# Kernel optimization log

Hardware: AMD Instinct MI355X
Metric: run time of the kernel (lower is better)

The kernel has to match this reference:

```python
import jax, jax.numpy as jnp
import numpy as np

NUM_HEADS = 16
ROPE_THETA = 10000.0
SEQ = 2048
D_MODEL = 2048


def _rope(x):
    # x: (seq, heads, head_dim). Equinox RotaryPositionalEmbedding:
    # rotate_half variant with tiled (non-interleaved) cos/sin.
    S, H, hd = x.shape
    half = hd // 2
    freqs = 1.0 / (ROPE_THETA ** (jnp.arange(0, half, dtype=jnp.float32) * 2.0 / hd))  # (half,)
    t = jnp.arange(S, dtype=jnp.float32)
    angles = jnp.outer(t, freqs)  # (S, half)
    cos = jnp.tile(jnp.cos(angles), (1, 2))[:, None, :]  # (S, 1, hd)
    sin = jnp.tile(jnp.sin(angles), (1, 2))[:, None, :]
    x1, x2 = jnp.split(x, 2, axis=-1)
    rot = jnp.concatenate((-x2, x1), axis=-1)  # rotate_half
    return (x * cos + rot * sin).astype(x.dtype)


def setup_inputs() -> dict:
    key = jax.random.key(0)
    ks = jax.random.split(key, 7)
    mk = lambda k, scale=1.0: (jax.random.normal(k, (SEQ, D_MODEL), dtype=jnp.float32) * scale)
    return {
        "query": mk(ks[0]),
        "key_": mk(ks[1]),
        "value": mk(ks[2]),
        "Wq": jax.random.normal(ks[3], (D_MODEL, D_MODEL), dtype=jnp.float32) / np.sqrt(D_MODEL),
        "Wk": jax.random.normal(ks[4], (D_MODEL, D_MODEL), dtype=jnp.float32) / np.sqrt(D_MODEL),
        "Wv": jax.random.normal(ks[5], (D_MODEL, D_MODEL), dtype=jnp.float32) / np.sqrt(D_MODEL),
        "Wo": jax.random.normal(ks[6], (D_MODEL, D_MODEL), dtype=jnp.float32) / np.sqrt(D_MODEL),
    }


def reference(query, key_, value, Wq, Wk, Wv, Wo):
    S, D = query.shape
    H = NUM_HEADS
    hd = D // H
    # QKV projections (equinox Linear: y = W @ x, vmapped over seq -> x @ W.T)
    q = (query @ Wq.T).reshape(S, H, hd)
    k = (key_ @ Wk.T).reshape(S, H, hd)
    v = (value @ Wv.T).reshape(S, H, hd)
    # Per-head RoPE on q and k
    q = _rope(q)
    k = _rope(k)
    # Causal attention, scale 1/sqrt(head_dim) (dropout_p=0, inference)
    attn = jax.nn.dot_product_attention(q[None], k[None], v[None], is_causal=True)[0]  # (S, H, hd)
    # Output projection
    return attn.reshape(S, D) @ Wo.T
```

## Files before the change

kernel.cpp:

```cpp
#include <hip/hip_runtime.h>

typedef unsigned short u16;
typedef __attribute__((ext_vector_type(8))) __bf16 bf16x8;
typedef __attribute__((ext_vector_type(4))) float f32x4;

#define D_MODEL 2048
#define SEQ 2048
#define NHEAD 16
#define HDIM 128

#define AS1 __attribute__((address_space(1)))
#define AS3 __attribute__((address_space(3)))
#define GL2LDS(g, l) __builtin_amdgcn_global_load_lds((AS1 const void*)(g), (AS3 void*)(l), 16, 0, 0)

__device__ __forceinline__ u16 f2bf(float f) {
  unsigned u = __float_as_uint(f);
  u += 0x7fff + ((u >> 16) & 1);
  return (u16)(u >> 16);
}
__device__ __forceinline__ float bf2f(u16 h) {
  return __uint_as_float(((unsigned)h) << 16);
}
__device__ __forceinline__ float fexp2(float x) {
#if __has_builtin(__builtin_amdgcn_exp2f)
  return __builtin_amdgcn_exp2f(x);
#else
  return __expf(x * 0.69314718055994531f);
#endif
}

__global__ __launch_bounds__(256) void k_cast7(const float* i0, const float* i1, const float* i2,
                                               const float* i3, const float* i4, const float* i5,
                                               const float* i6,
                                               u16* o0, u16* o1, u16* o2, u16* o3, u16* o4,
                                               u16* o5, u16* o6) {
  const float* in; u16* out;
  switch (blockIdx.y) {
    case 0: in = i0; out = o0; break;
    case 1: in = i1; out = o1; break;
    case 2: in = i2; out = o2; break;
    case 3: in = i3; out = o3; break;
    case 4: in = i4; out = o4; break;
    case 5: in = i5; out = o5; break;
    default: in = i6; out = o6; break;
  }
  const int i = blockIdx.x * blockDim.x + threadIdx.x;
  const float4 v = reinterpret_cast<const float4*>(in)[i];
  ushort4 o;
  o.x = f2bf(v.x); o.y = f2bf(v.y); o.z = f2bf(v.z); o.w = f2bf(v.w);
  reinterpret_cast<ushort4*>(out)[i] = o;
}

__device__ __forceinline__ void stage128(const u16* __restrict__ P, u16* dst, int row0, int kt,
                                         int t, int w) {
#pragma unroll
  for (int c = 0; c < 4; ++c) {
    const int r = (c * 2048 + t * 8) >> 6;
    const int ch = ((t & 7) ^ (r & 7)) * 8;
    GL2LDS(P + (size_t)(row0 + r) * D_MODEL + kt + ch, dst + c * 2048 + w * 512);
  }
}
__device__ __forceinline__ void stage64(const u16* __restrict__ P, u16* dst, int row0, int kt,
                                        int t, int w) {
#pragma unroll
  for (int c = 0; c < 2; ++c) {
    const int r = (c * 2048 + t * 8) >> 6;
    const int ch = ((t & 7) ^ (r & 7)) * 8;
    GL2LDS(P + (size_t)(row0 + r) * D_MODEL + kt + ch, dst + c * 2048 + w * 512);
  }
}

__device__ __forceinline__ void gemm_nt_body(const u16* __restrict__ A, const u16* __restrict__ B,
                                             void* __restrict__ C, u16* As0, u16* As1,
                                             u16* Bs0, u16* Bs1, int outmode) {
  const int tn = blockIdx.x, tm = blockIdx.y;
  const int t = threadIdx.x;
  const int lane = t & 63, w = t >> 6;
  const int wr = w >> 1, wc = w & 1;
  const int lrow = lane & 15, g = lane >> 4;
  f32x4 acc[4][4] = {};

  stage128(A, As0, tm * 128, 0, t, w);
  stage128(B, Bs0, tn * 128, 0, t, w);
  __syncthreads();

  u16 *Ar = As0, *Br = Bs0, *Aw = As1, *Bw = Bs1;
#pragma unroll 1
  for (int kt = 0; kt < D_MODEL; kt += 64) {
    if (kt + 64 < D_MODEL) {
      stage128(A, Aw, tm * 128, kt + 64, t, w);
      stage128(B, Bw, tn * 128, kt + 64, t, w);
    }
#pragma unroll
    for (int kk = 0; kk < 2; ++kk) {
      bf16x8 af[4], bfr[4];
#pragma unroll
      for (int i = 0; i < 4; ++i) {
        const int sw = (((kk << 2) + g) ^ (lrow & 7)) * 8;
        af[i]  = *(const bf16x8*)(Ar + (wr * 64 + i * 16 + lrow) * 64 + sw);
        bfr[i] = *(const bf16x8*)(Br + (wc * 64 + i * 16 + lrow) * 64 + sw);
      }
#pragma unroll
      for (int i = 0; i < 4; ++i)
#pragma unroll
        for (int j = 0; j < 4; ++j)
          acc[i][j] = __builtin_amdgcn_mfma_f32_16x16x32_bf16(af[i], bfr[j], acc[i][j], 0, 0, 0);
    }
    __syncthreads();
    u16* tp;
    tp = Ar; Ar = Aw; Aw = tp;
    tp = Br; Br = Bw; Bw = tp;
  }

  const int crow0 = tm * 128 + wr * 64 + (lane >> 4) * 4;
  const int ccol0 = tn * 128 + wc * 64 + lrow;
  if (outmode == 2) {
#pragma unroll
    for (int i = 0; i < 4; ++i)
#pragma unroll
      for (int j = 0; j < 4; ++j) {
        ushort4 o;
        o.x = f2bf(acc[i][j][0]); o.y = f2bf(acc[i][j][1]);
        o.z = f2bf(acc[i][j][2]); o.w = f2bf(acc[i][j][3]);
        *(ushort4*)((u16*)C + (size_t)(ccol0 + j * 16) * D_MODEL + crow0 + i * 16) = o;
      }
  } else {
#pragma unroll
    for (int i = 0; i < 4; ++i)
#pragma unroll
      for (int j = 0; j < 4; ++j)
#pragma unroll
        for (int r = 0; r < 4; ++r)
          ((u16*)C)[(size_t)(crow0 + i * 16 + r) * D_MODEL + ccol0 + j * 16] = f2bf(acc[i][j][r]);
  }
}

__global__ __launch_bounds__(256, 2) void k_gemm_qkv(const u16* Xq, const u16* Xk, const u16* Xv,
                                                     const u16* Wq, const u16* Wk, const u16* Wv,
                                                     u16* Q, u16* K, u16* VT) {
  __shared__ u16 As[2][128 * 64], Bs[2][128 * 64];
  const int z = blockIdx.z;
  const u16* A = (z == 0) ? Xq : (z == 1) ? Xk : Xv;
  const u16* B = (z == 0) ? Wq : (z == 1) ? Wk : Wv;
  u16* C = (z == 0) ? Q : (z == 1) ? K : VT;
  gemm_nt_body(A, B, C, As[0], As[1], Bs[0], Bs[1], (z == 2) ? 2 : 0);
}

__global__ __launch_bounds__(256, 2) void k_gemm_out(const u16* __restrict__ A, const u16* __restrict__ B,
                                                     float* __restrict__ C) {
  __shared__ u16 As[2][128 * 64], Bs[2][64 * 64];
  const int tn = blockIdx.x, tm = blockIdx.y;
  const int t = threadIdx.x;
  const int lane = t & 63, w = t >> 6;
  const int wr = w >> 1, wc = w & 1;
  const int lrow = lane & 15, g = lane >> 4;
  f32x4 acc[4][2] = {};

  stage128(A, As[0], tm * 128, 0, t, w);
  stage64(B, Bs[0], tn * 64, 0, t, w);
  __syncthreads();

  u16 *Ar = As[0], *Br = Bs[0], *Aw = As[1], *Bw = Bs[1];
#pragma unroll 1
  for (int kt = 0; kt < D_MODEL; kt += 64) {
    if (kt + 64 < D_MODEL) {
      stage128(A, Aw, tm * 128, kt + 64, t, w);
      stage64(B, Bw, tn * 64, kt + 64, t, w);
    }
#pragma unroll
    for (int kk = 0; kk < 2; ++kk) {
      bf16x8 af[4], bfr[2];
#pragma unroll
      for (int i = 0; i < 4; ++i) {
        const int sw = (((kk << 2) + g) ^ (lrow & 7)) * 8;
        af[i] = *(const bf16x8*)(Ar + (wr * 64 + i * 16 + lrow) * 64 + sw);
        if (i < 2) bfr[i] = *(const bf16x8*)(Br + (wc * 32 + i * 16 + lrow) * 64 + sw);
      }
#pragma unroll
      for (int i = 0; i < 4; ++i)
#pragma unroll
        for (int j = 0; j < 2; ++j)
          acc[i][j] = __builtin_amdgcn_mfma_f32_16x16x32_bf16(af[i], bfr[j], acc[i][j], 0, 0, 0);
    }
    __syncthreads();
    u16* tp;
    tp = Ar; Ar = Aw; Aw = tp;
    tp = Br; Br = Bw; Bw = tp;
  }
  const int crow0 = tm * 128 + wr * 64 + (lane >> 4) * 4;
  const int ccol0 = tn * 64 + wc * 32 + lrow;
#pragma unroll
  for (int i = 0; i < 4; ++i)
#pragma unroll
    for (int j = 0; j < 2; ++j)
#pragma unroll
      for (int r = 0; r < 4; ++r)
        C[(size_t)(crow0 + i * 16 + r) * D_MODEL + ccol0 + j * 16] = acc[i][j][r];
}

__global__ __launch_bounds__(256) void k_rope(u16* Q, u16* K) {
  const int idx = blockIdx.x * blockDim.x + threadIdx.x;
  u16* X = blockIdx.y ? K : Q;
  const float scale = blockIdx.y ? 1.0f : (1.4426950408889634f * 0.08838834764831845f);
  const int s = idx >> 10;
  const int h = (idx >> 6) & 15;
  const int j = idx & 63;
  const float freq = __expf((float)j * -0.14391156831212787f);
  float sn, cs;
  sincosf((float)s * freq, &sn, &cs);
  const size_t base = (size_t)s * D_MODEL + h * HDIM + j;
  const float x1 = bf2f(X[base]), x2 = bf2f(X[base + 64]);
  X[base]      = f2bf((x1 * cs - x2 * sn) * scale);
  X[base + 64] = f2bf((x2 * cs + x1 * sn) * scale);
}

__global__ __launch_bounds__(256) void k_attn(const u16* __restrict__ Q, const u16* __restrict__ K,
                                              const u16* __restrict__ VT, u16* __restrict__ O) {
  __shared__ u16 Kb[2][2][64 * 128];
  __shared__ u16 Vb[2][2][128 * 64];
  __shared__ u16 Pl[4][32 * 64];
  const int bx = blockIdx.x;
  const int h = bx & 15;
  const int pj = bx >> 4;
  const int t = threadIdx.x;
  const int lane = t & 63, w = t >> 6;
  const int mh = w & 1, par = w >> 1;
  const int lrow = lane & 15, g = lane >> 4, lk = g * 8;

  auto STAGE = [&](int b, int ss, int nt2) {
    const int t0 = 2 * ss;
    const int t1 = (2 * ss + 1 < nt2) ? 2 * ss + 1 : nt2 - 1;
#pragma unroll
    for (int i = 0; i < 4; ++i) {
      const int rk = w * 16 + i * 4 + (lane >> 4);
      const int ck = lane & 15;
      GL2LDS(K + (size_t)(t0 * 64 + rk) * D_MODEL + h * HDIM + ((ck ^ (rk & 15)) * 8),
             Kb[b][0] + (w * 16 + i * 4) * 128);
      GL2LDS(K + (size_t)(t1 * 64 + rk) * D_MODEL + h * HDIM + ((ck ^ (rk & 15)) * 8),
             Kb[b][1] + (w * 16 + i * 4) * 128);
      const int rv = w * 32 + i * 8 + (lane >> 3);
      const int cv = lane & 7;
      GL2LDS(VT + (size_t)(h * HDIM + rv) * D_MODEL + t0 * 64 + ((cv ^ (rv & 7)) * 8),
             Vb[b][0] + (w * 32 + i * 8) * 64);
      GL2LDS(VT + (size_t)(h * HDIM + rv) * D_MODEL + t1 * 64 + ((cv ^ (rv & 7)) * 8),
             Vb[b][1] + (w * 32 + i * 8) * 64);
    }
  };

  int cur = 0;
#pragma unroll 1
  for (int side = 0; side < 2; ++side) {
    const int qt = side ? (31 - pj) : pj;
    const int nt = qt + 1;
    const int nss = (nt + 1) >> 1;
    const int qrow0 = qt * 64 + mh * 32;

    bf16x8 qf[2][4];
#pragma unroll
    for (int mi = 0; mi < 2; ++mi)
#pragma unroll
      for (int ks = 0; ks < 4; ++ks)
        qf[mi][ks] = *(const bf16x8*)(Q + (size_t)(qrow0 + mi * 16 + lrow) * D_MODEL + h * HDIM + ks * 32 + lk);

    f32x4 accO[2][8] = {};
    float m_run[2][4], l_run[2][4];
#pragma unroll
    for (int mi = 0; mi < 2; ++mi)
#pragma unroll
      for (int r = 0; r < 4; ++r) { m_run[mi][r] = -1e30f; l_run[mi][r] = 0.f; }

    STAGE(cur, 0, nt);
    __syncthreads();

#pragma unroll 1
    for (int ss = 0; ss < nss; ++ss) {
      if (ss + 1 < nss) STAGE(cur ^ 1, ss + 1, nt);

      const int T = 2 * ss + par;
      if (T < nt) {
        f32x4 sc[2][4] = {};
#pragma unroll
        for (int ks = 0; ks < 4; ++ks) {
          bf16x8 kf[4];
#pragma unroll
          for (int ni = 0; ni < 4; ++ni)
            kf[ni] = *(const bf16x8*)(&Kb[cur][par][(ni * 16 + lrow) * 128 + ((ks * 4 + g) ^ lrow) * 8]);
#pragma unroll
          for (int mi = 0; mi < 2; ++mi)
#pragma unroll
            for (int ni = 0; ni < 4; ++ni)
              sc[mi][ni] = __builtin_amdgcn_mfma_f32_16x16x32_bf16(qf[mi][ks], kf[ni], sc[mi][ni], 0, 0, 0);
        }

        if (T == qt) {
          const int kv = T * 64;
#pragma unroll
          for (int mi = 0; mi < 2; ++mi)
#pragma unroll
            for (int ni = 0; ni < 4; ++ni) {
              const int colg = kv + ni * 16 + lrow;
#pragma unroll
              for (int r = 0; r < 4; ++r) {
                const int rowg = qrow0 + mi * 16 + g * 4 + r;
                if (colg > rowg) sc[mi][ni][r] = -1e30f;
              }
            }
        }

#pragma unroll
        for (int mi = 0; mi < 2; ++mi)
#pragma unroll
          for (int r = 0; r < 4; ++r) {
            float pm = fmaxf(fmaxf(sc[mi][0][r], sc[mi][1][r]), fmaxf(sc[mi][2][r], sc[mi][3][r]));
            pm = fmaxf(pm, __shfl_xor(pm, 1));
            pm = fmaxf(pm, __shfl_xor(pm, 2));
            pm = fmaxf(pm, __shfl_xor(pm, 4));
            pm = fmaxf(pm, __shfl_xor(pm, 8));
            const float mo = m_run[mi][r];
            const bool defer = __all(pm - mo <= 8.f);
            float base = mo, sf = 1.0f;
            if (!defer) {
              base = fmaxf(mo, pm);
              sf = fexp2(mo - base);
              m_run[mi][r] = base;
            }
            float rs = 0.f;
#pragma unroll
            for (int ni = 0; ni < 4; ++ni) {
              const float p = fexp2(sc[mi][ni][r] - base);
              sc[mi][ni][r] = p;
              rs += p;
            }
            rs += __shfl_xor(rs, 1);
            rs += __shfl_xor(rs, 2);
            rs += __shfl_xor(rs, 4);
            rs += __shfl_xor(rs, 8);
            l_run[mi][r] = fmaf(l_run[mi][r], sf, rs);
            if (!defer) {
#pragma unroll
              for (int dt = 0; dt < 8; ++dt) accO[mi][dt][r] *= sf;
            }
          }

#pragma unroll
        for (int mi = 0; mi < 2; ++mi)
#pragma unroll
          for (int ni = 0; ni < 4; ++ni)
#pragma unroll
            for (int r = 0; r < 4; ++r) {
              const int row = mi * 16 + g * 4 + r;
              const int chnk = (2 * ni + (lrow >> 3)) ^ (row & 7);
              Pl[w][row * 64 + chnk * 8 + (lrow & 7)] = f2bf(sc[mi][ni][r]);
            }
        asm volatile("s_waitcnt lgkmcnt(0)" ::: "memory");

#pragma unroll
        for (int ks2 = 0; ks2 < 2; ++ks2) {
          bf16x8 pf[2];
#pragma unroll
          for (int mi = 0; mi < 2; ++mi) {
            const int row = mi * 16 + lrow;
            pf[mi] = *(const bf16x8*)(&Pl[w][row * 64 + ((ks2 * 4 + g) ^ (row & 7)) * 8]);
          }
#pragma unroll
          for (int dt = 0; dt < 8; ++dt) {
            const int R = dt * 16 + lrow;
            const bf16x8 vf = *(const bf16x8*)(&Vb[cur][par][R * 64 + ((ks2 * 4 + g) ^ (R & 7)) * 8]);
#pragma unroll
            for (int mi = 0; mi < 2; ++mi)
              accO[mi][dt] = __builtin_amdgcn_mfma_f32_16x16x32_bf16(pf[mi], vf, accO[mi][dt], 0, 0, 0);
          }
        }
      }
      __syncthreads();
      cur ^= 1;
    }

    float* mrg = (float*)&Kb[0][0][0];
    float* mlb = (float*)&Vb[0][0][0];
    if (par == 1) {
#pragma unroll
      for (int mi = 0; mi < 2; ++mi)
#pragma unroll
        for (int dt = 0; dt < 8; ++dt)
#pragma unroll
          for (int r = 0; r < 4; ++r)
            mrg[mh * 4096 + (mi * 16 + g * 4 + r) * 128 + dt * 16 + lrow] = accO[mi][dt][r];
#pragma unroll
      for (int mi = 0; mi < 2; ++mi)
#pragma unroll
        for (int r = 0; r < 4; ++r) {
          const int row = mi * 16 + g * 4 + r;
          mlb[mh * 64 + row * 2]     = m_run[mi][r];
          mlb[mh * 64 + row * 2 + 1] = l_run[mi][r];
        }
    }
    __syncthreads();
    if (par == 0) {
#pragma unroll
      for (int mi = 0; mi < 2; ++mi)
#pragma unroll
        for (int r = 0; r < 4; ++r) {
          const int row = mi * 16 + g * 4 + r;
          const float m1 = mlb[mh * 64 + row * 2];
          const float l1 = mlb[mh * 64 + row * 2 + 1];
          const float mn = fmaxf(m_run[mi][r], m1);
          const float f0 = fexp2(m_run[mi][r] - mn);
          const float f1 = fexp2(m1 - mn);
          const float inv = 1.0f / (l_run[mi][r] * f0 + l1 * f1);
          const size_t grow = (size_t)(qrow0 + row);
#pragma unroll
          for (int dt = 0; dt < 8; ++dt) {
            const float v1 = mrg[mh * 4096 + row * 128 + dt * 16 + lrow];
            O[grow * D_MODEL + h * HDIM + dt * 16 + lrow] =
                f2bf((accO[mi][dt][r] * f0 + v1 * f1) * inv);
          }
        }
    }
    __syncthreads();
  }
}

extern "C" void kernel_launch(void* const* d_in, const int* in_sizes, int n_in,
                              void* d_out, int out_size, void* d_ws, size_t ws_size,
                              hipStream_t stream) {
  const float* query = (const float*)d_in[0];
  const float* key_  = (const float*)d_in[1];
  const float* value = (const float*)d_in[2];
  const float* Wq    = (const float*)d_in[3];
  const float* Wk    = (const float*)d_in[4];
  const float* Wv    = (const float*)d_in[5];
  const float* Wo    = (const float*)d_in[6];
  float* out = (float*)d_out;

  const size_t TS = (size_t)SEQ * D_MODEL;
  u16* ws  = (u16*)d_ws;
  u16* bXq = ws + 0 * TS;
  u16* bXk = ws + 1 * TS;
  u16* bXv = ws + 2 * TS;
  u16* bWq = ws + 3 * TS;
  u16* bWk = ws + 4 * TS;
  u16* bWv = ws + 5 * TS;
  u16* bWo = ws + 6 * TS;
  u16* bQ  = ws + 7 * TS;
  u16* bK  = ws + 8 * TS;
  u16* bVT = ws + 9 * TS;
  u16* bA  = ws + 10 * TS;

  const int n4 = (int)(TS / 4);
  k_cast7<<<dim3(n4 / 256, 7), 256, 0, stream>>>(query, key_, value, Wq, Wk, Wv, Wo,
                                                 bXq, bXk, bXv, bWq, bWk, bWv, bWo);

  k_gemm_qkv<<<dim3(16, 16, 3), 256, 0, stream>>>(bXq, bXk, bXv, bWq, bWk, bWv, bQ, bK, bVT);

  k_rope<<<dim3((SEQ * NHEAD * 64) / 256, 2), 256, 0, stream>>>(bQ, bK);

  k_attn<<<dim3(256), 256, 0, stream>>>(bQ, bK, bVT, bA);

  k_gemm_out<<<dim3(32, 16), 256, 0, stream>>>(bA, bWo, out);
}
```

Baseline: 343.0 us.

## Process both causal query tiles concurrently in 512-thread attention blocks sharing KV loads

The attention kernel now launches 512 threads per block. Four waves handle the short-side query tile and four handle the long-side tile, and both consume the same staged K/V tiles instead of looping over the two sides one after the other. The QK and PV MFMAs are transposed so each lane owns one query row. That makes softmax reductions cheaper (two shuffles) and allows vectorized P writes and output stores. The cost is that the K/V double buffering is removed, so loads are no longer overlapped with compute and there is a sync per step. Short-side waves also sit idle for most iterations.

```diff
diff --git a/kernel.cpp b/kernel.cpp
--- a/kernel.cpp
+++ b/kernel.cpp
@@ -214,210 +214,198 @@
   X[base + 64] = f2bf((x2 * cs + x1 * sn) * scale);
 }
 
-__global__ __launch_bounds__(256) void k_attn(const u16* __restrict__ Q, const u16* __restrict__ K,
+__global__ __launch_bounds__(512) void k_attn(const u16* __restrict__ Q, const u16* __restrict__ K,
                                               const u16* __restrict__ VT, u16* __restrict__ O) {
-  __shared__ u16 Kb[2][2][64 * 128];
-  __shared__ u16 Vb[2][2][128 * 64];
-  __shared__ u16 Pl[4][32 * 64];
+  __shared__ u16 Kb[2][64 * 128];
+  __shared__ u16 Vb[2][128 * 64];
+  __shared__ u16 Pl[8][32 * 64];
   const int bx = blockIdx.x;
   const int h = bx & 15;
   const int pj = bx >> 4;
   const int t = threadIdx.x;
   const int lane = t & 63, w = t >> 6;
-  const int mh = w & 1, par = w >> 1;
+  const int side = w >> 2;
+  const int par = (w >> 1) & 1;
+  const int mh = w & 1;
   const int lrow = lane & 15, g = lane >> 4, lk = g * 8;
-
-  auto STAGE = [&](int b, int ss, int nt2) {
+  const int qt = side ? (31 - pj) : pj;
+  const int nt = qt + 1;
+  const int qrow0 = qt * 64 + mh * 32;
+  const int ntB = 32 - pj;
+  const int nss = (ntB + 1) >> 1;
+
+  bf16x8 qf[2][4];
+#pragma unroll
+  for (int mi = 0; mi < 2; ++mi)
+#pragma unroll
+    for (int ks = 0; ks < 4; ++ks)
+      qf[mi][ks] = *(const bf16x8*)(Q + (size_t)(qrow0 + mi * 16 + lrow) * D_MODEL + h * HDIM + ks * 32 + lk);
+
+  f32x4 accO[2][8] = {};
+  float m_run[2] = {-1e30f, -1e30f};
+  float l_run[2] = {0.f, 0.f};
+
+#pragma unroll 1
+  for (int ss = 0; ss < nss; ++ss) {
     const int t0 = 2 * ss;
-    const int t1 = (2 * ss + 1 < nt2) ? 2 * ss + 1 : nt2 - 1;
+    const int t1 = (2 * ss + 1 < ntB) ? 2 * ss + 1 : ntB - 1;
 #pragma unroll
     for (int i = 0; i < 4; ++i) {
-      const int rk = w * 16 + i * 4 + (lane >> 4);
-      const int ck = lane & 15;
-      GL2LDS(K + (size_t)(t0 * 64 + rk) * D_MODEL + h * HDIM + ((ck ^ (rk & 15)) * 8),
-             Kb[b][0] + (w * 16 + i * 4) * 128);
-      GL2LDS(K + (size_t)(t1 * 64 + rk) * D_MODEL + h * HDIM + ((ck ^ (rk & 15)) * 8),
-             Kb[b][1] + (w * 16 + i * 4) * 128);
-      const int rv = w * 32 + i * 8 + (lane >> 3);
-      const int cv = lane & 7;
-      GL2LDS(VT + (size_t)(h * HDIM + rv) * D_MODEL + t0 * 64 + ((cv ^ (rv & 7)) * 8),
-             Vb[b][0] + (w * 32 + i * 8) * 64);
-      GL2LDS(VT + (size_t)(h * HDIM + rv) * D_MODEL + t1 * 64 + ((cv ^ (rv & 7)) * 8),
-             Vb[b][1] + (w * 32 + i * 8) * 64);
-    }
-  };
-
-  int cur = 0;
-#pragma unroll 1
-  for (int side = 0; side < 2; ++side) {
-    const int qt = side ? (31 - pj) : pj;
-    const int nt = qt + 1;
-    const int nss = (nt + 1) >> 1;
-    const int qrow0 = qt * 64 + mh * 32;
-
-    bf16x8 qf[2][4];
-#pragma unroll
-    for (int mi = 0; mi < 2; ++mi)
-#pragma unroll
-      for (int ks = 0; ks < 4; ++ks)
-        qf[mi][ks] = *(const bf16x8*)(Q + (size_t)(qrow0 + mi * 16 + lrow) * D_MODEL + h * HDIM + ks * 32 + lk);
-
-    f32x4 accO[2][8] = {};
-    float m_run[2][4], l_run[2][4];
-#pragma unroll
-    for (int mi = 0; mi < 2; ++mi)
-#pragma unroll
-      for (int r = 0; r < 4; ++r) { m_run[mi][r] = -1e30f; l_run[mi][r] = 0.f; }
-
-    STAGE(cur, 0, nt);
+      {
+        const int idx = i * 512 + t;
+        const int tl = idx >> 10, row = (idx >> 4) & 63, ck = idx & 15;
+        GL2LDS(K + (size_t)((tl ? t1 : t0) * 64 + row) * D_MODEL + h * HDIM + ((ck ^ (row & 15)) * 8),
+               Kb[0] + idx * 8);
+      }
+      {
+        const int idx = i * 512 + t;
+        const int tl = idx >> 10, row = (idx >> 3) & 127, cv = idx & 7;
+        GL2LDS(VT + (size_t)(h * HDIM + row) * D_MODEL + (tl ? t1 : t0) * 64 + ((cv ^ (row & 7)) * 8),
+               Vb[0] + idx * 8);
+      }
+    }
     __syncthreads();
 
-#pragma unroll 1
-    for (int ss = 0; ss < nss; ++ss) {
-      if (ss + 1 < nss) STAGE(cur ^ 1, ss + 1, nt);
-
-      const int T = 2 * ss + par;
-      if (T < nt) {
-        f32x4 sc[2][4] = {};
-#pragma unroll
-        for (int ks = 0; ks < 4; ++ks) {
-          bf16x8 kf[4];
-#pragma unroll
-          for (int ni = 0; ni < 4; ++ni)
-            kf[ni] = *(const bf16x8*)(&Kb[cur][par][(ni * 16 + lrow) * 128 + ((ks * 4 + g) ^ lrow) * 8]);
+    const int T = 2 * ss + par;
+    if (T < nt) {
+      f32x4 scs[4][2] = {};
+#pragma unroll
+      for (int ks = 0; ks < 4; ++ks) {
+        bf16x8 kf[4];
+#pragma unroll
+        for (int kb = 0; kb < 4; ++kb)
+          kf[kb] = *(const bf16x8*)(&Kb[par][(kb * 16 + lrow) * 128 + ((ks * 4 + g) ^ lrow) * 8]);
+#pragma unroll
+        for (int kb = 0; kb < 4; ++kb)
 #pragma unroll
           for (int mi = 0; mi < 2; ++mi)
-#pragma unroll
-            for (int ni = 0; ni < 4; ++ni)
-              sc[mi][ni] = __builtin_amdgcn_mfma_f32_16x16x32_bf16(qf[mi][ks], kf[ni], sc[mi][ni], 0, 0, 0);
-        }
-
-        if (T == qt) {
-          const int kv = T * 64;
-#pragma unroll
-          for (int mi = 0; mi < 2; ++mi)
-#pragma unroll
-            for (int ni = 0; ni < 4; ++ni) {
-              const int colg = kv + ni * 16 + lrow;
-#pragma unroll
-              for (int r = 0; r < 4; ++r) {
-                const int rowg = qrow0 + mi * 16 + g * 4 + r;
-                if (colg > rowg) sc[mi][ni][r] = -1e30f;
-              }
-            }
-        }
-
-#pragma unroll
-        for (int mi = 0; mi < 2; ++mi)
-#pragma unroll
-          for (int r = 0; r < 4; ++r) {
-            float pm = fmaxf(fmaxf(sc[mi][0][r], sc[mi][1][r]), fmaxf(sc[mi][2][r], sc[mi][3][r]));
-            pm = fmaxf(pm, __shfl_xor(pm, 1));
-            pm = fmaxf(pm, __shfl_xor(pm, 2));
-            pm = fmaxf(pm, __shfl_xor(pm, 4));
-            pm = fmaxf(pm, __shfl_xor(pm, 8));
-            const float mo = m_run[mi][r];
-            const bool defer = __all(pm - mo <= 8.f);
-            float base = mo, sf = 1.0f;
-            if (!defer) {
-              base = fmaxf(mo, pm);
-              sf = fexp2(mo - base);
-              m_run[mi][r] = base;
-            }
-            float rs = 0.f;
-#pragma unroll
-            for (int ni = 0; ni < 4; ++ni) {
-              const float p = fexp2(sc[mi][ni][r] - base);
-              sc[mi][ni][r] = p;
-              rs += p;
-            }
-            rs += __shfl_xor(rs, 1);
-            rs += __shfl_xor(rs, 2);
-            rs += __shfl_xor(rs, 4);
-            rs += __shfl_xor(rs, 8);
-            l_run[mi][r] = fmaf(l_run[mi][r], sf, rs);
-            if (!defer) {
-#pragma unroll
-              for (int dt = 0; dt < 8; ++dt) accO[mi][dt][r] *= sf;
+            scs[kb][mi] = __builtin_amdgcn_mfma_f32_16x16x32_bf16(kf[kb], qf[mi][ks], scs[kb][mi], 0, 0, 0);
+      }
+
+      if (T == qt) {
+#pragma unroll
+        for (int kb = 0; kb < 4; ++kb)
+#pragma unroll
+          for (int mi = 0; mi < 2; ++mi) {
+            const int qg = qrow0 + mi * 16 + lrow;
+#pragma unroll
+            for (int r = 0; r < 4; ++r) {
+              const int kvg = T * 64 + kb * 16 + g * 4 + r;
+              if (kvg > qg) scs[kb][mi][r] = -1e30f;
             }
           }
-
-#pragma unroll
-        for (int mi = 0; mi < 2; ++mi)
-#pragma unroll
-          for (int ni = 0; ni < 4; ++ni)
-#pragma unroll
-            for (int r = 0; r < 4; ++r) {
-              const int row = mi * 16 + g * 4 + r;
-              const int chnk = (2 * ni + (lrow >> 3)) ^ (row & 7);
-              Pl[w][row * 64 + chnk * 8 + (lrow & 7)] = f2bf(sc[mi][ni][r]);
-            }
-        asm volatile("s_waitcnt lgkmcnt(0)" ::: "memory");
-
-#pragma unroll
-        for (int ks2 = 0; ks2 < 2; ++ks2) {
-          bf16x8 pf[2];
-#pragma unroll
-          for (int mi = 0; mi < 2; ++mi) {
-            const int row = mi * 16 + lrow;
-            pf[mi] = *(const bf16x8*)(&Pl[w][row * 64 + ((ks2 * 4 + g) ^ (row & 7)) * 8]);
+      }
+
+#pragma unroll
+      for (int mi = 0; mi < 2; ++mi) {
+        float pm = -1e30f;
+#pragma unroll
+        for (int kb = 0; kb < 4; ++kb)
+#pragma unroll
+          for (int r = 0; r < 4; ++r) pm = fmaxf(pm, scs[kb][mi][r]);
+        pm = fmaxf(pm, __shfl_xor(pm, 16));
+        pm = fmaxf(pm, __shfl_xor(pm, 32));
+        const float mo = m_run[mi];
+        const bool defer = __all(pm - mo <= 8.f);
+        float base = mo, sf = 1.0f;
+        if (!defer) {
+          base = fmaxf(mo, pm);
+          sf = fexp2(mo - base);
+          m_run[mi] = base;
+        }
+        float rs = 0.f;
+#pragma unroll
+        for (int kb = 0; kb < 4; ++kb)
+#pragma unroll
+          for (int r = 0; r < 4; ++r) {
+            const float p = fexp2(scs[kb][mi][r] - base);
+            scs[kb][mi][r] = p;
+            rs += p;
           }
-#pragma unroll
-          for (int dt = 0; dt < 8; ++dt) {
-            const int R = dt * 16 + lrow;
-            const bf16x8 vf = *(const bf16x8*)(&Vb[cur][par][R * 64 + ((ks2 * 4 + g) ^ (R & 7)) * 8]);
-#pragma unroll
-            for (int mi = 0; mi < 2; ++mi)
-              accO[mi][dt] = __builtin_amdgcn_mfma_f32_16x16x32_bf16(pf[mi], vf, accO[mi][dt], 0, 0, 0);
-          }
+        rs += __shfl_xor(rs, 16);
+        rs += __shfl_xor(rs, 32);
+        l_run[mi] = fmaf(l_run[mi], sf, rs);
+        if (!defer) {
+#pragma unroll
+          for (int dt = 0; dt < 8; ++dt)
+#pragma unroll
+            for (int r = 0; r < 4; ++r) accO[mi][dt][r] *= sf;
         }
       }
-      __syncthreads();
-      cur ^= 1;
-    }
-
-    float* mrg = (float*)&Kb[0][0][0];
-    float* mlb = (float*)&Vb[0][0][0];
-    if (par == 1) {
-#pragma unroll
-      for (int mi = 0; mi < 2; ++mi)
-#pragma unroll
-        for (int dt = 0; dt < 8; ++dt)
-#pragma unroll
-          for (int r = 0; r < 4; ++r)
-            mrg[mh * 4096 + (mi * 16 + g * 4 + r) * 128 + dt * 16 + lrow] = accO[mi][dt][r];
-#pragma unroll
-      for (int mi = 0; mi < 2; ++mi)
-#pragma unroll
-        for (int r = 0; r < 4; ++r) {
-          const int row = mi * 16 + g * 4 + r;
-          mlb[mh * 64 + row * 2]     = m_run[mi][r];
-          mlb[mh * 64 + row * 2 + 1] = l_run[mi][r];
+
+#pragma unroll
+      for (int mi = 0; mi < 2; ++mi) {
+        const int row = mi * 16 + lrow;
+#pragma unroll
+        for (int kb = 0; kb < 4; ++kb) {
+          ushort4 o;
+          o.x = f2bf(scs[kb][mi][0]); o.y = f2bf(scs[kb][mi][1]);
+          o.z = f2bf(scs[kb][mi][2]); o.w = f2bf(scs[kb][mi][3]);
+          *(ushort4*)(&Pl[w][row * 64 + (((kb << 1) + (g >> 1)) ^ (row & 7)) * 8 + (g & 1) * 4]) = o;
         }
+      }
+      asm volatile("s_waitcnt lgkmcnt(0)" ::: "memory");
+      __builtin_amdgcn_sched_barrier(0);
+
+#pragma unroll
+      for (int ks2 = 0; ks2 < 2; ++ks2) {
+        bf16x8 pf[2];
+#pragma unroll
+        for (int mi = 0; mi < 2; ++mi) {
+          const int row = mi * 16 + lrow;
+          pf[mi] = *(const bf16x8*)(&Pl[w][row * 64 + ((ks2 * 4 + g) ^ (row & 7)) * 8]);
+        }
+#pragma unroll
+        for (int dt = 0; dt < 8; ++dt) {
+          const int R = dt * 16 + lrow;
+          const bf16x8 vf = *(const bf16x8*)(&Vb[par][R * 64 + ((ks2 * 4 + g) ^ (R & 7)) * 8]);
+#pragma unroll
+          for (int mi = 0; mi < 2; ++mi)
+            accO[mi][dt] = __builtin_amdgcn_mfma_f32_16x16x32_bf16(vf, pf[mi], accO[mi][dt], 0, 0, 0);
+        }
+      }
     }
     __syncthreads();
-    if (par == 0) {
-#pragma unroll
-      for (int mi = 0; mi < 2; ++mi)
-#pragma unroll
-        for (int r = 0; r < 4; ++r) {
-          const int row = mi * 16 + g * 4 + r;
-          const float m1 = mlb[mh * 64 + row * 2];
-          const float l1 = mlb[mh * 64 + row * 2 + 1];
-          const float mn = fmaxf(m_run[mi][r], m1);
-          const float f0 = fexp2(m_run[mi][r] - mn);
-          const float f1 = fexp2(m1 - mn);
-          const float inv = 1.0f / (l_run[mi][r] * f0 + l1 * f1);
-          const size_t grow = (size_t)(qrow0 + row);
-#pragma unroll
-          for (int dt = 0; dt < 8; ++dt) {
-            const float v1 = mrg[mh * 4096 + row * 128 + dt * 16 + lrow];
-            O[grow * D_MODEL + h * HDIM + dt * 16 + lrow] =
-                f2bf((accO[mi][dt][r] * f0 + v1 * f1) * inv);
-          }
-        }
-    }
-    __syncthreads();
+  }
+
+  float* mrg = side ? (float*)&Vb[0][0] : (float*)&Kb[0][0];
+  float* mlb = (float*)&Pl[0][0] + side * 128;
+  if (par == 1) {
+#pragma unroll
+    for (int mi = 0; mi < 2; ++mi) {
+      const int ql = mi * 16 + lrow;
+#pragma unroll
+      for (int dt = 0; dt < 8; ++dt)
+        *(f32x4*)(&mrg[mh * 4096 + ql * 128 + dt * 16 + g * 4]) = accO[mi][dt];
+      if (g == 0) {
+        mlb[mh * 64 + ql * 2]     = m_run[mi];
+        mlb[mh * 64 + ql * 2 + 1] = l_run[mi];
+      }
+    }
+  }
+  __syncthreads();
+  if (par == 0) {
+#pragma unroll
+    for (int mi = 0; mi < 2; ++mi) {
+      const int ql = mi * 16 + lrow;
+      const float m1 = mlb[mh * 64 + ql * 2];
+      const float l1 = mlb[mh * 64 + ql * 2 + 1];
+      const float mn = fmaxf(m_run[mi], m1);
+      const float f0 = fexp2(m_run[mi] - mn);
+      const float f1 = fexp2(m1 - mn);
+      const float inv = 1.0f / (l_run[mi] * f0 + l1 * f1);
+      const size_t grow = (size_t)(qrow0 + ql);
+#pragma unroll
+      for (int dt = 0; dt < 8; ++dt) {
+        const f32x4 v1 = *(const f32x4*)(&mrg[mh * 4096 + ql * 128 + dt * 16 + g * 4]);
+        ushort4 o;
+        o.x = f2bf((accO[mi][dt][0] * f0 + v1[0] * f1) * inv);
+        o.y = f2bf((accO[mi][dt][1] * f0 + v1[1] * f1) * inv);
+        o.z = f2bf((accO[mi][dt][2] * f0 + v1[2] * f1) * inv);
+        o.w = f2bf((accO[mi][dt][3] * f0 + v1[3] * f1) * inv);
+        *(ushort4*)(&O[grow * D_MODEL + h * HDIM + dt * 16 + g * 4]) = o;
+      }
+    }
   }
 }
 
@@ -455,7 +443,7 @@
 
   k_rope<<<dim3((SEQ * NHEAD * 64) / 256, 2), 256, 0, stream>>>(bQ, bK);
 
-  k_attn<<<dim3(256), 256, 0, stream>>>(bQ, bK, bVT, bA);
+  k_attn<<<dim3(256), 512, 0, stream>>>(bQ, bK, bVT, bA);
 
   k_gemm_out<<<dim3(32, 16), 256, 0, stream>>>(bA, bWo, out);
 }
```

Measured after the change: 290.0 us. -15.4%, faster.
